# Kernel optimization log

Hardware: AMD Instinct MI355X
Metric: run time of the kernel (lower is better)

The kernel has to match this reference:

```python
import jax, jax.numpy as jnp
import numpy as np

B, F, V, E, D1, DD, L2 = 4096, 32, 50000, 64, 256, 16, 128


def setup_inputs() -> dict:
    key = jax.random.key(0)
    ks = jax.random.split(key, 16)
    s = 0.05  # small init scale to keep tanh unsaturated
    return {
        "sparse": jax.random.randint(ks[0], (B, F), 0, V, dtype=jnp.int32),
        "dense": jax.random.normal(ks[1], (B, DD), dtype=jnp.float32),
        "tables": jax.random.normal(ks[2], (F, V, E), dtype=jnp.float32) * s,
        "Wz": jax.random.normal(ks[3], (D1, F, E), dtype=jnp.float32) * s,
        "bz": jnp.zeros((D1,), jnp.float32),
        "Wpi": jax.random.normal(ks[4], (D1, F, F), dtype=jnp.float32) * s,
        "bpi": jnp.zeros((D1,), jnp.float32),
        "Wpo": jax.random.normal(ks[5], (D1, E, E), dtype=jnp.float32) * s,
        "bpo": jnp.zeros((D1,), jnp.float32),
        "B1": jax.random.normal(ks[6], (D1,), dtype=jnp.float32) * s,
        "W1": jax.random.normal(ks[7], (D1 + DD, D1), dtype=jnp.float32) * s,
        "b1": jnp.zeros((D1,), jnp.float32),
        "W2": jax.random.normal(ks[8], (D1, L2), dtype=jnp.float32) * s,
        "b2": jnp.zeros((L2,), jnp.float32),
        "W3": jax.random.normal(ks[9], (L2, 1), dtype=jnp.float32) * s,
        "b3": jnp.zeros((1,), jnp.float32),
    }


def reference(sparse, dense, tables, Wz, bz, Wpi, bpi, Wpo, bpo, B1,
              W1, b1, W2, b2, W3, b3):
    # Embedding lookup: per-field table gather -> [B, F, E]
    emb = tables[jnp.arange(F)[None, :], sparse]
    # Lz: Conv1d(in=F, kernel=E) over [B, F, E] == full contraction -> [B, D1]
    Lz = jnp.einsum('bfe,dfe->bd', emb, Wz) + bz
    # Inner product: [B, F, F], then Conv1d(in=F, kernel=F) full contraction
    inner = jnp.einsum('bie,bje->bij', emb, emb)
    Lp_inner = jnp.einsum('bij,dij->bd', inner, Wpi) + bpi
    # Outer product: sum_{i,j} x_i^T x_j == s^T s with s = sum_i x_i (exact rewrite)
    s = emb.sum(axis=1)                      # [B, E]
    outer = s[:, :, None] * s[:, None, :]    # [B, E, E]
    Lp_outer = jnp.einsum('bij,dij->bd', outer, Wpo) + bpo
    L1 = Lz + Lp_inner + Lp_outer + B1       # [B, D1]
    deep_x = jnp.concatenate([L1, dense], axis=1)  # [B, D1+DD]
    h = jnp.tanh(deep_x @ W1 + b1)
    h = jnp.tanh(h @ W2 + b2)
    out = (h @ W3 + b3)[:, 0]                # [B]
    return out
```

## Files before the change

### kernel.cpp

```cpp
#include <hip/hip_runtime.h>
#include <hip/hip_bf16.h>

#define B_    4096
#define F_    32
#define V_    50000
#define E_    64
#define D1_   256
#define DD_   16
#define L2N_  128
#define KX    3072
#define KTOT  7168
#define NKC   8

typedef __bf16 bf16x8 __attribute__((ext_vector_type(8)));
typedef float  f32x4  __attribute__((ext_vector_type(4)));

typedef __attribute__((address_space(1))) const void gvoid;
typedef __attribute__((address_space(3))) void svoid;

__device__ __forceinline__ ushort f2b(float f){
  __bf16 h = (__bf16)f; return __builtin_bit_cast(ushort, h);
}
__device__ __forceinline__ float b2f(ushort u){
  return __uint_as_float(((uint)u) << 16);
}
__device__ __forceinline__ float blo(uint u){ return __uint_as_float(u << 16); }
__device__ __forceinline__ float bhi(uint u){ return __uint_as_float(u & 0xffff0000u); }
__device__ __forceinline__ void gload16(const void* g, void* l){
  __builtin_amdgcn_global_load_lds((gvoid*)g, (svoid*)l, 16, 0, 0);
}

__global__ __launch_bounds__(256) void prep_gather(
    const float* __restrict__ Wz, const float* __restrict__ Wpi,
    const float* __restrict__ Wpo, const float* __restrict__ W1,
    const float* __restrict__ W2,
    const int* __restrict__ sparse, const float* __restrict__ tables,
    ushort* __restrict__ WBb, ushort* __restrict__ W1b, ushort* __restrict__ W2b,
    ushort* __restrict__ Xb, ushort* __restrict__ Sb) {
  __shared__ ushort gsh[4][32 * 72];
  int bid = blockIdx.x, t = threadIdx.x;
  if (bid < 640) {
    if (bid < 256) {
      int n = bid;
#pragma unroll
      for (int j = 0; j < 7; ++j) {
        int k4 = (j * 256 + t) * 4;
        float4 v;
        if (k4 < 2048)      v = *(const float4*)&Wz [(size_t)n * 2048 + k4];
        else if (k4 < 3072) v = *(const float4*)&Wpi[(size_t)n * 1024 + (k4 - 2048)];
        else                v = *(const float4*)&Wpo[(size_t)n * 4096 + (k4 - 3072)];
        ushort4 o = make_ushort4(f2b(v.x), f2b(v.y), f2b(v.z), f2b(v.w));
        *(ushort4*)&WBb[(size_t)n * KTOT + k4] = o;
      }
    } else if (bid < 512) {
      int n = bid - 256;
      float v0 = (t < 272) ? W1[(size_t)t * 256 + n] : 0.f;
      W1b[(size_t)n * 288 + t] = f2b(v0);
      if (t < 32) {
        int k2 = 256 + t;
        float v1 = (k2 < 272) ? W1[(size_t)k2 * 256 + n] : 0.f;
        W1b[(size_t)n * 288 + k2] = f2b(v1);
      }
    } else {
      int n = bid - 512;
      W2b[(size_t)n * 256 + t] = f2b(W2[(size_t)t * 128 + n]);
    }
    return;
  }

  int w = t >> 6, l = t & 63;
  int b = (bid - 640) * 4 + w;
  int fr = l & 15, q = l >> 4;

  int i0 = sparse[b * F_ + fr];
  int i1 = sparse[b * F_ + 16 + fr];
  const float* r0 = tables + ((size_t)fr * V_ + i0) * 64;
  const float* r1 = tables + ((size_t)(16 + fr) * V_ + i1) * 64;

  float4 v[2][2][2];
#pragma unroll
  for (int ks = 0; ks < 2; ++ks) {
    v[0][ks][0] = *(const float4*)(r0 + ks * 32 + q * 8);
    v[0][ks][1] = *(const float4*)(r0 + ks * 32 + q * 8 + 4);
    v[1][ks][0] = *(const float4*)(r1 + ks * 32 + q * 8);
    v[1][ks][1] = *(const float4*)(r1 + ks * 32 + q * 8 + 4);
  }

  bf16x8 fg[2][2];
#pragma unroll
  for (int rh = 0; rh < 2; ++rh)
#pragma unroll
    for (int ks = 0; ks < 2; ++ks) {
      bf16x8 a;
      a[0] = (__bf16)v[rh][ks][0].x; a[1] = (__bf16)v[rh][ks][0].y;
      a[2] = (__bf16)v[rh][ks][0].z; a[3] = (__bf16)v[rh][ks][0].w;
      a[4] = (__bf16)v[rh][ks][1].x; a[5] = (__bf16)v[rh][ks][1].y;
      a[6] = (__bf16)v[rh][ks][1].z; a[7] = (__bf16)v[rh][ks][1].w;
      fg[rh][ks] = a;
      *(bf16x8*)&Xb[(size_t)b * KX + (rh * 16 + fr) * 64 + ks * 32 + q * 8] = a;
    }

  float sv[2][8];
#pragma unroll
  for (int ks = 0; ks < 2; ++ks) {
    sv[ks][0] = v[0][ks][0].x + v[1][ks][0].x; sv[ks][1] = v[0][ks][0].y + v[1][ks][0].y;
    sv[ks][2] = v[0][ks][0].z + v[1][ks][0].z; sv[ks][3] = v[0][ks][0].w + v[1][ks][0].w;
    sv[ks][4] = v[0][ks][1].x + v[1][ks][1].x; sv[ks][5] = v[0][ks][1].y + v[1][ks][1].y;
    sv[ks][6] = v[0][ks][1].z + v[1][ks][1].z; sv[ks][7] = v[0][ks][1].w + v[1][ks][1].w;
  }
#pragma unroll
  for (int m = 1; m < 16; m <<= 1)
#pragma unroll
    for (int ks = 0; ks < 2; ++ks)
#pragma unroll
      for (int j = 0; j < 8; ++j)
        sv[ks][j] += __shfl_xor(sv[ks][j], m, 64);
  if (fr == 0) {
#pragma unroll
    for (int ks = 0; ks < 2; ++ks) {
      ushort4 o0 = make_ushort4(f2b(sv[ks][0]), f2b(sv[ks][1]), f2b(sv[ks][2]), f2b(sv[ks][3]));
      ushort4 o1 = make_ushort4(f2b(sv[ks][4]), f2b(sv[ks][5]), f2b(sv[ks][6]), f2b(sv[ks][7]));
      *(ushort4*)&Sb[(size_t)b * 64 + ks * 32 + q * 8]     = o0;
      *(ushort4*)&Sb[(size_t)b * 64 + ks * 32 + q * 8 + 4] = o1;
    }
  }

  f32x4 g[2][2] = {};
#pragma unroll
  for (int ks = 0; ks < 2; ++ks)
#pragma unroll
    for (int ri = 0; ri < 2; ++ri)
#pragma unroll
      for (int rj = 0; rj < 2; ++rj)
        g[ri][rj] = __builtin_amdgcn_mfma_f32_16x16x32_bf16(
            fg[ri][ks], fg[rj][ks], g[ri][rj], 0, 0, 0);

#pragma unroll
  for (int ri = 0; ri < 2; ++ri)
#pragma unroll
    for (int rj = 0; rj < 2; ++rj)
#pragma unroll
      for (int r = 0; r < 4; ++r)
        gsh[w][(ri * 16 + q * 4 + r) * 72 + rj * 16 + fr] = f2b(g[ri][rj][r]);
  {
    int rrow = l >> 1, rcol = (l & 1) * 16;
    uint4 ga = *(const uint4*)&gsh[w][rrow * 72 + rcol];
    uint4 gb = *(const uint4*)&gsh[w][rrow * 72 + rcol + 8];
    size_t dst = (size_t)b * KX + 2048 + rrow * 32 + rcol;
    *(uint4*)&Xb[dst]     = ga;
    *(uint4*)&Xb[dst + 8] = gb;
  }
}

__global__ __launch_bounds__(512, 1) void gemm_l1(
    const ushort* __restrict__ Xb, const ushort* __restrict__ WBb,
    const ushort* __restrict__ Sb, ushort* __restrict__ Lp) {
  __shared__ __align__(16) ushort As[2][128 * 64];
  __shared__ __align__(16) ushort Bs[2][256 * 64];
  __shared__ ushort Ssl[128 * 18];

  int bid = blockIdx.x;
  int kc  = bid & 7;
  int mT  = bid >> 3;
  int bRow = mT * 128;
  int kt0 = kc * 14;
  int i_start = min(max(0, kt0 - 48), 48);

  int tid = threadIdx.x, w = tid >> 6, l = tid & 63;
  int wm = (w >> 2) * 64, wn = (w & 3) * 64;
  int fr = l & 15, q = l >> 4;

#pragma unroll
  for (int r = 0; r < 2; ++r) {
    int p = r * 1024 + tid * 2;
    int row = p >> 4, col = p & 15;
    *(ushort2*)&Ssl[row * 18 + col] =
        *(const ushort2*)&Sb[(size_t)(bRow + row) * 64 + i_start + col];
  }

  uint4 sregu[4][2];
#pragma unroll
  for (int mi = 0; mi < 4; ++mi) {
    int grow = bRow + wm + mi * 16 + fr;
    sregu[mi][0] = *(const uint4*)&Sb[(size_t)grow * 64 + q * 8];
    sregu[mi][1] = *(const uint4*)&Sb[(size_t)grow * 64 + 32 + q * 8];
  }

  int r8 = l >> 3;
  int sg = ((l & 7) ^ r8) * 8;

  auto stageA = [&](int bI, int kt) {
    const ushort* src = Xb + (size_t)(bRow + w * 16 + r8) * KX + kt * 64 + sg;
#pragma unroll
    for (int c = 0; c < 2; ++c)
      gload16(src + (size_t)(c * 8) * KX, &As[bI][(w * 16 + c * 8) * 64]);
  };
  auto stageB = [&](int bI, int kt) {
    const ushort* src = WBb + (size_t)(w * 32 + r8) * KTOT + kt * 64 + sg;
#pragma unroll
    for (int c = 0; c < 4; ++c)
      gload16(src + (size_t)(c * 8) * KTOT, &Bs[bI][(w * 32 + c * 8) * 64]);
  };

  f32x4 acc[4][4] = {};
  bf16x8 af[4][2], bfr[4][2];
  int buf = 0;

  if (kt0 < 48) stageA(0, kt0);
  stageB(0, kt0);
  __syncthreads();

#pragma unroll
  for (int tl = 0; tl < 14; ++tl) {
    int kt = kt0 + tl;
    if (tl + 1 < 14) {
      if (kt + 1 < 48) stageA(buf ^ 1, kt + 1);
      stageB(buf ^ 1, kt + 1);
    }

#pragma unroll
    for (int ni = 0; ni < 4; ++ni) {
      int col = wn + ni * 16 + fr;
#pragma unroll
      for (int ks = 0; ks < 2; ++ks) {
        int slot = (ks * 4 + q) ^ (col & 7);
        bfr[ni][ks] = *(const bf16x8*)&Bs[buf][col * 64 + slot * 8];
      }
    }
    if (kt < 48) {
#pragma unroll
      for (int mi = 0; mi < 4; ++mi) {
        int row = wm + mi * 16 + fr;
#pragma unroll
        for (int ks = 0; ks < 2; ++ks) {
          int slot = (ks * 4 + q) ^ (row & 7);
          af[mi][ks] = *(const bf16x8*)&As[buf][row * 64 + slot * 8];
        }
      }
    } else {
      int iloc = kt - 48 - i_start;
#pragma unroll
      for (int mi = 0; mi < 4; ++mi) {
        float si = b2f(Ssl[(wm + mi * 16 + fr) * 18 + iloc]);
#pragma unroll
        for (int ks = 0; ks < 2; ++ks) {
          uint4 uv = sregu[mi][ks];
          bf16x8 a;
          a[0] = (__bf16)(si * blo(uv.x)); a[1] = (__bf16)(si * bhi(uv.x));
          a[2] = (__bf16)(si * blo(uv.y)); a[3] = (__bf16)(si * bhi(uv.y));
          a[4] = (__bf16)(si * blo(uv.z)); a[5] = (__bf16)(si * bhi(uv.z));
          a[6] = (__bf16)(si * blo(uv.w)); a[7] = (__bf16)(si * bhi(uv.w));
          af[mi][ks] = a;
        }
      }
    }
#pragma unroll
    for (int ks = 0; ks < 2; ++ks)
#pragma unroll
      for (int mi = 0; mi < 4; ++mi)
#pragma unroll
        for (int ni = 0; ni < 4; ++ni)
          acc[mi][ni] = __builtin_amdgcn_mfma_f32_16x16x32_bf16(
              af[mi][ks], bfr[ni][ks], acc[mi][ni], 0, 0, 0);
    __syncthreads();
    buf ^= 1;
  }

  ushort* Lpk = Lp + (size_t)kc * (B_ * D1_);
#pragma unroll
  for (int mi = 0; mi < 4; ++mi) {
    int row0 = bRow + wm + mi * 16 + q * 4;
#pragma unroll
    for (int ni = 0; ni < 4; ++ni) {
      int col = wn + ni * 16 + fr;
#pragma unroll
      for (int r = 0; r < 4; ++r)
        Lpk[(size_t)(row0 + r) * D1_ + col] = f2b(acc[mi][ni][r]);
    }
  }
}

__global__ __launch_bounds__(256) void mlp_fused(
    const ushort* __restrict__ Lp, const float* __restrict__ dense,
    const ushort* __restrict__ W1b, const ushort* __restrict__ W2b,
    const float* __restrict__ bz, const float* __restrict__ bpi,
    const float* __restrict__ bpo, const float* __restrict__ B1v,
    const float* __restrict__ b1, const float* __restrict__ b2,
    const float* __restrict__ W3, const float* __restrict__ b3,
    float* __restrict__ out) {
  __shared__ ushort hs[16 * 264];
  __shared__ ushort h2s[16 * 136];
  __shared__ float bvs[256];
  int b0 = blockIdx.x * 16;
  int tid = threadIdx.x, w = tid >> 6, l = tid & 63;
  int row = l & 15, q = l >> 4;
  int wn = w * 64;

  bvs[tid] = bz[tid] + bpi[tid] + bpo[tid] + B1v[tid];
  __syncthreads();

  f32x4 acc1[4] = {};
  for (int kt = 0; kt < 9; ++kt) {
    int k0 = kt * 32 + q * 8;
    bf16x8 afr;
    if (kt < 8) {
      size_t base = (size_t)(b0 + row) * D1_ + k0;
      float s[8] = {0.f, 0.f, 0.f, 0.f, 0.f, 0.f, 0.f, 0.f};
#pragma unroll
      for (int p = 0; p < NKC; ++p) {
        uint4 u = *(const uint4*)&Lp[(size_t)p * (B_ * D1_) + base];
        s[0] += blo(u.x); s[1] += bhi(u.x);
        s[2] += blo(u.y); s[3] += bhi(u.y);
        s[4] += blo(u.z); s[5] += bhi(u.z);
        s[6] += blo(u.w); s[7] += bhi(u.w);
      }
      float4 bv0 = *(const float4*)&bvs[k0];
      float4 bv1 = *(const float4*)&bvs[k0 + 4];
      afr[0] = (__bf16)(s[0] + bv0.x); afr[1] = (__bf16)(s[1] + bv0.y);
      afr[2] = (__bf16)(s[2] + bv0.z); afr[3] = (__bf16)(s[3] + bv0.w);
      afr[4] = (__bf16)(s[4] + bv1.x); afr[5] = (__bf16)(s[5] + bv1.y);
      afr[6] = (__bf16)(s[6] + bv1.z); afr[7] = (__bf16)(s[7] + bv1.w);
    } else if (q < 2) {
      float4 u0 = *(const float4*)&dense[(size_t)(b0 + row) * DD_ + q * 8];
      float4 u1 = *(const float4*)&dense[(size_t)(b0 + row) * DD_ + q * 8 + 4];
      afr[0] = (__bf16)u0.x; afr[1] = (__bf16)u0.y; afr[2] = (__bf16)u0.z; afr[3] = (__bf16)u0.w;
      afr[4] = (__bf16)u1.x; afr[5] = (__bf16)u1.y; afr[6] = (__bf16)u1.z; afr[7] = (__bf16)u1.w;
    } else {
      afr = (bf16x8)(__bf16)0.f;
    }
#pragma unroll
    for (int ni = 0; ni < 4; ++ni) {
      bf16x8 bfr = *(const bf16x8*)&W1b[(size_t)(wn + ni * 16 + row) * 288 + k0];
      acc1[ni] = __builtin_amdgcn_mfma_f32_16x16x32_bf16(afr, bfr, acc1[ni], 0, 0, 0);
    }
  }
#pragma unroll
  for (int ni = 0; ni < 4; ++ni) {
    int col = wn + ni * 16 + row;
    float bias = b1[col];
#pragma unroll
    for (int r = 0; r < 4; ++r)
      hs[(q * 4 + r) * 264 + col] = f2b(tanhf(acc1[ni][r] + bias));
  }
  __syncthreads();

  int wn2 = w * 32;
  f32x4 acc2[2] = {};
  for (int kt = 0; kt < 8; ++kt) {
    int k0 = kt * 32 + q * 8;
    bf16x8 afr = *(const bf16x8*)&hs[row * 264 + k0];
#pragma unroll
    for (int ni = 0; ni < 2; ++ni) {
      bf16x8 bfr = *(const bf16x8*)&W2b[(size_t)(wn2 + ni * 16 + row) * 256 + k0];
      acc2[ni] = __builtin_amdgcn_mfma_f32_16x16x32_bf16(afr, bfr, acc2[ni], 0, 0, 0);
    }
  }
#pragma unroll
  for (int ni = 0; ni < 2; ++ni) {
    int col = wn2 + ni * 16 + row;
    float bias = b2[col];
#pragma unroll
    for (int r = 0; r < 4; ++r)
      h2s[(q * 4 + r) * 136 + col] = f2b(tanhf(acc2[ni][r] + bias));
  }
  __syncthreads();

  if (w == 0) {
    int rr = l >> 2, g = l & 3;
    float sum = 0.f;
#pragma unroll
    for (int jj = 0; jj < 32; ++jj) {
      int j = g * 32 + jj;
      sum += b2f(h2s[rr * 136 + j]) * W3[j];
    }
    sum += __shfl_xor(sum, 1, 64);
    sum += __shfl_xor(sum, 2, 64);
    if (g == 0) out[b0 + rr] = sum + b3[0];
  }
}

extern "C" void kernel_launch(void* const* d_in, const int* in_sizes, int n_in,
                              void* d_out, int out_size, void* d_ws, size_t ws_size,
                              hipStream_t stream) {
  const int*   sparse = (const int*)  d_in[0];
  const float* dense  = (const float*)d_in[1];
  const float* tables = (const float*)d_in[2];
  const float* Wz     = (const float*)d_in[3];
  const float* bz     = (const float*)d_in[4];
  const float* Wpi    = (const float*)d_in[5];
  const float* bpi    = (const float*)d_in[6];
  const float* Wpo    = (const float*)d_in[7];
  const float* bpo    = (const float*)d_in[8];
  const float* B1v    = (const float*)d_in[9];
  const float* W1     = (const float*)d_in[10];
  const float* b1     = (const float*)d_in[11];
  const float* W2     = (const float*)d_in[12];
  const float* b2     = (const float*)d_in[13];
  const float* W3     = (const float*)d_in[14];
  const float* b3     = (const float*)d_in[15];
  float* out = (float*)d_out;

  char* ws = (char*)d_ws;
  ushort* Xb  = (ushort*)(ws);
  ushort* WBb = (ushort*)(ws + 25165824);
  ushort* W1b = (ushort*)(ws + 28835840);
  ushort* W2b = (ushort*)(ws + 28983296);
  ushort* Sb  = (ushort*)(ws + 29048832);
  ushort* Lp  = (ushort*)(ws + 29573120);

  prep_gather<<<dim3(1664), dim3(256), 0, stream>>>(
      Wz, Wpi, Wpo, W1, W2, sparse, tables, WBb, W1b, W2b, Xb, Sb);
  gemm_l1    <<<dim3(256),  dim3(512), 0, stream>>>(Xb, WBb, Sb, Lp);
  mlp_fused  <<<dim3(256),  dim3(256), 0, stream>>>(
      Lp, dense, W1b, W2b, bz, bpi, bpo, B1v, b1, b2, W3, b3, out);
}
```

Baseline: 59.77 us.

## Fuse MLP into split-K GEMM using per-tile atomic counter barrier

```diff
diff --git a/kernel.cpp b/kernel.cpp
--- a/kernel.cpp
+++ b/kernel.cpp
@@ -36,12 +36,14 @@
     const float* __restrict__ W2,
     const int* __restrict__ sparse, const float* __restrict__ tables,
     ushort* __restrict__ WBb, ushort* __restrict__ W1b, ushort* __restrict__ W2b,
-    ushort* __restrict__ Xb, ushort* __restrict__ Sb) {
+    ushort* __restrict__ Xb, ushort* __restrict__ Sb, int* __restrict__ cnt) {
   __shared__ ushort gsh[4][32 * 72];
   int bid = blockIdx.x, t = threadIdx.x;
-  if (bid < 640) {
-    if (bid < 256) {
-      int n = bid;
+  if (bid >= 1024) {
+    int bid2 = bid - 1024;
+    if (bid2 == 0 && t < 32) cnt[t] = 0;
+    if (bid2 < 256) {
+      int n = bid2;
 #pragma unroll
       for (int j = 0; j < 7; ++j) {
         int k4 = (j * 256 + t) * 4;
@@ -52,8 +54,8 @@
         ushort4 o = make_ushort4(f2b(v.x), f2b(v.y), f2b(v.z), f2b(v.w));
         *(ushort4*)&WBb[(size_t)n * KTOT + k4] = o;
       }
-    } else if (bid < 512) {
-      int n = bid - 256;
+    } else if (bid2 < 512) {
+      int n = bid2 - 256;
       float v0 = (t < 272) ? W1[(size_t)t * 256 + n] : 0.f;
       W1b[(size_t)n * 288 + t] = f2b(v0);
       if (t < 32) {
@@ -62,14 +64,14 @@
         W1b[(size_t)n * 288 + k2] = f2b(v1);
       }
     } else {
-      int n = bid - 512;
+      int n = bid2 - 512;
       W2b[(size_t)n * 256 + t] = f2b(W2[(size_t)t * 128 + n]);
     }
     return;
   }
 
   int w = t >> 6, l = t & 63;
-  int b = (bid - 640) * 4 + w;
+  int b = bid * 4 + w;
   int fr = l & 15, q = l >> 4;
 
   int i0 = sparse[b * F_ + fr];
@@ -152,9 +154,16 @@
   }
 }
 
-__global__ __launch_bounds__(512, 1) void gemm_l1(
+__global__ __launch_bounds__(512, 1) void gemm_mlp(
     const ushort* __restrict__ Xb, const ushort* __restrict__ WBb,
-    const ushort* __restrict__ Sb, ushort* __restrict__ Lp) {
+    const ushort* __restrict__ Sb, ushort* __restrict__ Lp,
+    const float* __restrict__ dense,
+    const ushort* __restrict__ W1b, const ushort* __restrict__ W2b,
+    const float* __restrict__ bz, const float* __restrict__ bpi,
+    const float* __restrict__ bpo, const float* __restrict__ B1v,
+    const float* __restrict__ b1, const float* __restrict__ b2,
+    const float* __restrict__ W3, const float* __restrict__ b3,
+    int* __restrict__ cnt, float* __restrict__ out) {
   __shared__ __align__(16) ushort As[2][128 * 64];
   __shared__ __align__(16) ushort Bs[2][256 * 64];
   __shared__ ushort Ssl[128 * 18];
@@ -278,104 +287,103 @@
         Lpk[(size_t)(row0 + r) * D1_ + col] = f2b(acc[mi][ni][r]);
     }
   }
-}
-
-__global__ __launch_bounds__(256) void mlp_fused(
-    const ushort* __restrict__ Lp, const float* __restrict__ dense,
-    const ushort* __restrict__ W1b, const ushort* __restrict__ W2b,
-    const float* __restrict__ bz, const float* __restrict__ bpi,
-    const float* __restrict__ bpo, const float* __restrict__ B1v,
-    const float* __restrict__ b1, const float* __restrict__ b2,
-    const float* __restrict__ W3, const float* __restrict__ b3,
-    float* __restrict__ out) {
-  __shared__ ushort hs[16 * 264];
-  __shared__ ushort h2s[16 * 136];
-  __shared__ float bvs[256];
-  int b0 = blockIdx.x * 16;
-  int tid = threadIdx.x, w = tid >> 6, l = tid & 63;
-  int row = l & 15, q = l >> 4;
-  int wn = w * 64;
-
-  bvs[tid] = bz[tid] + bpi[tid] + bpo[tid] + B1v[tid];
+
+  __threadfence();
+  if (tid == 0) {
+    atomicAdd(&cnt[mT], 1);
+    while (__hip_atomic_load(&cnt[mT], __ATOMIC_RELAXED,
+                             __HIP_MEMORY_SCOPE_AGENT) < NKC)
+      __builtin_amdgcn_s_sleep(8);
+  }
   __syncthreads();
-
-  f32x4 acc1[4] = {};
-  for (int kt = 0; kt < 9; ++kt) {
-    int k0 = kt * 32 + q * 8;
-    bf16x8 afr;
-    if (kt < 8) {
-      size_t base = (size_t)(b0 + row) * D1_ + k0;
-      float s[8] = {0.f, 0.f, 0.f, 0.f, 0.f, 0.f, 0.f, 0.f};
-#pragma unroll
-      for (int p = 0; p < NKC; ++p) {
-        uint4 u = *(const uint4*)&Lp[(size_t)p * (B_ * D1_) + base];
-        s[0] += blo(u.x); s[1] += bhi(u.x);
-        s[2] += blo(u.y); s[3] += bhi(u.y);
-        s[4] += blo(u.z); s[5] += bhi(u.z);
-        s[6] += blo(u.w); s[7] += bhi(u.w);
-      }
-      float4 bv0 = *(const float4*)&bvs[k0];
-      float4 bv1 = *(const float4*)&bvs[k0 + 4];
-      afr[0] = (__bf16)(s[0] + bv0.x); afr[1] = (__bf16)(s[1] + bv0.y);
-      afr[2] = (__bf16)(s[2] + bv0.z); afr[3] = (__bf16)(s[3] + bv0.w);
-      afr[4] = (__bf16)(s[4] + bv1.x); afr[5] = (__bf16)(s[5] + bv1.y);
-      afr[6] = (__bf16)(s[6] + bv1.z); afr[7] = (__bf16)(s[7] + bv1.w);
-    } else if (q < 2) {
-      float4 u0 = *(const float4*)&dense[(size_t)(b0 + row) * DD_ + q * 8];
-      float4 u1 = *(const float4*)&dense[(size_t)(b0 + row) * DD_ + q * 8 + 4];
-      afr[0] = (__bf16)u0.x; afr[1] = (__bf16)u0.y; afr[2] = (__bf16)u0.z; afr[3] = (__bf16)u0.w;
-      afr[4] = (__bf16)u1.x; afr[5] = (__bf16)u1.y; afr[6] = (__bf16)u1.z; afr[7] = (__bf16)u1.w;
-    } else {
-      afr = (bf16x8)(__bf16)0.f;
-    }
-#pragma unroll
-    for (int ni = 0; ni < 4; ++ni) {
-      bf16x8 bfr = *(const bf16x8*)&W1b[(size_t)(wn + ni * 16 + row) * 288 + k0];
-      acc1[ni] = __builtin_amdgcn_mfma_f32_16x16x32_bf16(afr, bfr, acc1[ni], 0, 0, 0);
-    }
-  }
-#pragma unroll
-  for (int ni = 0; ni < 4; ++ni) {
-    int col = wn + ni * 16 + row;
-    float bias = b1[col];
-#pragma unroll
-    for (int r = 0; r < 4; ++r)
-      hs[(q * 4 + r) * 264 + col] = f2b(tanhf(acc1[ni][r] + bias));
-  }
-  __syncthreads();
-
-  int wn2 = w * 32;
-  f32x4 acc2[2] = {};
-  for (int kt = 0; kt < 8; ++kt) {
-    int k0 = kt * 32 + q * 8;
-    bf16x8 afr = *(const bf16x8*)&hs[row * 264 + k0];
+  __threadfence();
+
+  {
+    ushort* hs  = &As[0][0];
+    ushort* h2s = &As[0][0] + 16 * 264;
+    float*  bvs = (float*)(&As[0][0] + 16 * 264 + 16 * 136);
+
+    int b0 = bRow + kc * 16;
+    int row = fr;
+
+    if (tid < 256) bvs[tid] = bz[tid] + bpi[tid] + bpo[tid] + B1v[tid];
+    __syncthreads();
+
+    int wn1 = w * 32;
+    f32x4 acc1[2] = {};
+    for (int kt = 0; kt < 9; ++kt) {
+      int k0 = kt * 32 + q * 8;
+      bf16x8 afr;
+      if (kt < 8) {
+        size_t base = (size_t)(b0 + row) * D1_ + k0;
+        float s[8] = {0.f, 0.f, 0.f, 0.f, 0.f, 0.f, 0.f, 0.f};
+#pragma unroll
+        for (int p = 0; p < NKC; ++p) {
+          uint4 u = *(const uint4*)&Lp[(size_t)p * (B_ * D1_) + base];
+          s[0] += blo(u.x); s[1] += bhi(u.x);
+          s[2] += blo(u.y); s[3] += bhi(u.y);
+          s[4] += blo(u.z); s[5] += bhi(u.z);
+          s[6] += blo(u.w); s[7] += bhi(u.w);
+        }
+        float4 bv0 = *(const float4*)&bvs[k0];
+        float4 bv1 = *(const float4*)&bvs[k0 + 4];
+        afr[0] = (__bf16)(s[0] + bv0.x); afr[1] = (__bf16)(s[1] + bv0.y);
+        afr[2] = (__bf16)(s[2] + bv0.z); afr[3] = (__bf16)(s[3] + bv0.w);
+        afr[4] = (__bf16)(s[4] + bv1.x); afr[5] = (__bf16)(s[5] + bv1.y);
+        afr[6] = (__bf16)(s[6] + bv1.z); afr[7] = (__bf16)(s[7] + bv1.w);
+      } else if (q < 2) {
+        float4 u0 = *(const float4*)&dense[(size_t)(b0 + row) * DD_ + q * 8];
+        float4 u1 = *(const float4*)&dense[(size_t)(b0 + row) * DD_ + q * 8 + 4];
+        afr[0] = (__bf16)u0.x; afr[1] = (__bf16)u0.y; afr[2] = (__bf16)u0.z; afr[3] = (__bf16)u0.w;
+        afr[4] = (__bf16)u1.x; afr[5] = (__bf16)u1.y; afr[6] = (__bf16)u1.z; afr[7] = (__bf16)u1.w;
+      } else {
+        afr = (bf16x8)(__bf16)0.f;
+      }
+#pragma unroll
+      for (int ni = 0; ni < 2; ++ni) {
+        bf16x8 bfr2 = *(const bf16x8*)&W1b[(size_t)(wn1 + ni * 16 + row) * 288 + k0];
+        acc1[ni] = __builtin_amdgcn_mfma_f32_16x16x32_bf16(afr, bfr2, acc1[ni], 0, 0, 0);
+      }
+    }
 #pragma unroll
     for (int ni = 0; ni < 2; ++ni) {
-      bf16x8 bfr = *(const bf16x8*)&W2b[(size_t)(wn2 + ni * 16 + row) * 256 + k0];
-      acc2[ni] = __builtin_amdgcn_mfma_f32_16x16x32_bf16(afr, bfr, acc2[ni], 0, 0, 0);
-    }
-  }
-#pragma unroll
-  for (int ni = 0; ni < 2; ++ni) {
-    int col = wn2 + ni * 16 + row;
-    float bias = b2[col];
-#pragma unroll
-    for (int r = 0; r < 4; ++r)
-      h2s[(q * 4 + r) * 136 + col] = f2b(tanhf(acc2[ni][r] + bias));
-  }
-  __syncthreads();
-
-  if (w == 0) {
-    int rr = l >> 2, g = l & 3;
-    float sum = 0.f;
-#pragma unroll
-    for (int jj = 0; jj < 32; ++jj) {
-      int j = g * 32 + jj;
-      sum += b2f(h2s[rr * 136 + j]) * W3[j];
-    }
-    sum += __shfl_xor(sum, 1, 64);
-    sum += __shfl_xor(sum, 2, 64);
-    if (g == 0) out[b0 + rr] = sum + b3[0];
+      int col = wn1 + ni * 16 + row;
+      float bias = b1[col];
+#pragma unroll
+      for (int r = 0; r < 4; ++r)
+        hs[(q * 4 + r) * 264 + col] = f2b(tanhf(acc1[ni][r] + bias));
+    }
+    __syncthreads();
+
+    int wn2 = w * 16;
+    f32x4 acc2 = {};
+    for (int kt = 0; kt < 8; ++kt) {
+      int k0 = kt * 32 + q * 8;
+      bf16x8 afr = *(const bf16x8*)&hs[row * 264 + k0];
+      bf16x8 bfr2 = *(const bf16x8*)&W2b[(size_t)(wn2 + row) * 256 + k0];
+      acc2 = __builtin_amdgcn_mfma_f32_16x16x32_bf16(afr, bfr2, acc2, 0, 0, 0);
+    }
+    {
+      int col = wn2 + row;
+      float bias = b2[col];
+#pragma unroll
+      for (int r = 0; r < 4; ++r)
+        h2s[(q * 4 + r) * 136 + col] = f2b(tanhf(acc2[r] + bias));
+    }
+    __syncthreads();
+
+    if (w == 0) {
+      int rr = l >> 2, g = l & 3;
+      float sum = 0.f;
+#pragma unroll
+      for (int jj = 0; jj < 32; ++jj) {
+        int j = g * 32 + jj;
+        sum += b2f(h2s[rr * 136 + j]) * W3[j];
+      }
+      sum += __shfl_xor(sum, 1, 64);
+      sum += __shfl_xor(sum, 2, 64);
+      if (g == 0) out[b0 + rr] = sum + b3[0];
+    }
   }
 }
 
@@ -407,10 +415,11 @@
   ushort* W2b = (ushort*)(ws + 28983296);
   ushort* Sb  = (ushort*)(ws + 29048832);
   ushort* Lp  = (ushort*)(ws + 29573120);
+  int*    cnt = (int*)   (ws + 46350336);
 
   prep_gather<<<dim3(1664), dim3(256), 0, stream>>>(
-      Wz, Wpi, Wpo, W1, W2, sparse, tables, WBb, W1b, W2b, Xb, Sb);
-  gemm_l1    <<<dim3(256),  dim3(512), 0, stream>>>(Xb, WBb, Sb, Lp);
-  mlp_fused  <<<dim3(256),  dim3(256), 0, stream>>>(
-      Lp, dense, W1b, W2b, bz, bpi, bpo, B1v, b1, b2, W3, b3, out);
-}
+      Wz, Wpi, Wpo, W1, W2, sparse, tables, WBb, W1b, W2b, Xb, Sb, cnt);
+  gemm_mlp   <<<dim3(256),  dim3(512), 0, stream>>>(
+      Xb, WBb, Sb, Lp, dense, W1b, W2b, bz, bpi, bpo, B1v,
+      b1, b2, W3, b3, cnt, out);
+}
```

New measurement: 169.7 us. 184% more time.

## Halve GEMM M-tile, cut K-split to four, map split-K chunks to XCDs

Applied to the files above, without the earlier changes.

```diff
diff --git a/kernel.cpp b/kernel.cpp
--- a/kernel.cpp
+++ b/kernel.cpp
@@ -10,7 +10,7 @@
 #define L2N_  128
 #define KX    3072
 #define KTOT  7168
-#define NKC   8
+#define NKC   4
 
 typedef __bf16 bf16x8 __attribute__((ext_vector_type(8)));
 typedef float  f32x4  __attribute__((ext_vector_type(4)));
@@ -39,9 +39,10 @@
     ushort* __restrict__ Xb, ushort* __restrict__ Sb) {
   __shared__ ushort gsh[4][32 * 72];
   int bid = blockIdx.x, t = threadIdx.x;
-  if (bid < 640) {
-    if (bid < 256) {
-      int n = bid;
+  if (bid >= 1024) {
+    int bid2 = bid - 1024;
+    if (bid2 < 256) {
+      int n = bid2;
 #pragma unroll
       for (int j = 0; j < 7; ++j) {
         int k4 = (j * 256 + t) * 4;
@@ -52,8 +53,8 @@
         ushort4 o = make_ushort4(f2b(v.x), f2b(v.y), f2b(v.z), f2b(v.w));
         *(ushort4*)&WBb[(size_t)n * KTOT + k4] = o;
       }
-    } else if (bid < 512) {
-      int n = bid - 256;
+    } else if (bid2 < 512) {
+      int n = bid2 - 256;
       float v0 = (t < 272) ? W1[(size_t)t * 256 + n] : 0.f;
       W1b[(size_t)n * 288 + t] = f2b(v0);
       if (t < 32) {
@@ -62,14 +63,14 @@
         W1b[(size_t)n * 288 + k2] = f2b(v1);
       }
     } else {
-      int n = bid - 512;
+      int n = bid2 - 512;
       W2b[(size_t)n * 256 + t] = f2b(W2[(size_t)t * 128 + n]);
     }
     return;
   }
 
   int w = t >> 6, l = t & 63;
-  int b = (bid - 640) * 4 + w;
+  int b = bid * 4 + w;
   int fr = l & 15, q = l >> 4;
 
   int i0 = sparse[b * F_ + fr];
@@ -155,32 +156,30 @@
 __global__ __launch_bounds__(512, 1) void gemm_l1(
     const ushort* __restrict__ Xb, const ushort* __restrict__ WBb,
     const ushort* __restrict__ Sb, ushort* __restrict__ Lp) {
-  __shared__ __align__(16) ushort As[2][128 * 64];
+  __shared__ __align__(16) ushort As[2][64 * 64];
   __shared__ __align__(16) ushort Bs[2][256 * 64];
-  __shared__ ushort Ssl[128 * 18];
+  __shared__ ushort Ssl[64 * 72];
 
   int bid = blockIdx.x;
-  int kc  = bid & 7;
-  int mT  = bid >> 3;
-  int bRow = mT * 128;
-  int kt0 = kc * 14;
-  int i_start = min(max(0, kt0 - 48), 48);
+  int xcd = bid & 7;
+  int kc  = xcd >> 1;
+  int mT  = (bid >> 3) * 2 + (xcd & 1);
+  int bRow = mT * 64;
+  int kt0 = kc * 28;
 
   int tid = threadIdx.x, w = tid >> 6, l = tid & 63;
-  int wm = (w >> 2) * 64, wn = (w & 3) * 64;
+  int wm = (w >> 2) * 32, wn = (w & 3) * 64;
   int fr = l & 15, q = l >> 4;
 
-#pragma unroll
-  for (int r = 0; r < 2; ++r) {
-    int p = r * 1024 + tid * 2;
-    int row = p >> 4, col = p & 15;
-    *(ushort2*)&Ssl[row * 18 + col] =
-        *(const ushort2*)&Sb[(size_t)(bRow + row) * 64 + i_start + col];
-  }
-
-  uint4 sregu[4][2];
-#pragma unroll
-  for (int mi = 0; mi < 4; ++mi) {
+  {
+    int p = tid * 8;
+    int row = p >> 6, col = p & 63;
+    *(uint4*)&Ssl[row * 72 + col] = *(const uint4*)&Sb[(size_t)(bRow + row) * 64 + col];
+  }
+
+  uint4 sregu[2][2];
+#pragma unroll
+  for (int mi = 0; mi < 2; ++mi) {
     int grow = bRow + wm + mi * 16 + fr;
     sregu[mi][0] = *(const uint4*)&Sb[(size_t)grow * 64 + q * 8];
     sregu[mi][1] = *(const uint4*)&Sb[(size_t)grow * 64 + 32 + q * 8];
@@ -190,10 +189,8 @@
   int sg = ((l & 7) ^ r8) * 8;
 
   auto stageA = [&](int bI, int kt) {
-    const ushort* src = Xb + (size_t)(bRow + w * 16 + r8) * KX + kt * 64 + sg;
-#pragma unroll
-    for (int c = 0; c < 2; ++c)
-      gload16(src + (size_t)(c * 8) * KX, &As[bI][(w * 16 + c * 8) * 64]);
+    const ushort* src = Xb + (size_t)(bRow + w * 8 + r8) * KX + kt * 64 + sg;
+    gload16(src, &As[bI][(w * 8) * 64]);
   };
   auto stageB = [&](int bI, int kt) {
     const ushort* src = WBb + (size_t)(w * 32 + r8) * KTOT + kt * 64 + sg;
@@ -202,8 +199,8 @@
       gload16(src + (size_t)(c * 8) * KTOT, &Bs[bI][(w * 32 + c * 8) * 64]);
   };
 
-  f32x4 acc[4][4] = {};
-  bf16x8 af[4][2], bfr[4][2];
+  f32x4 acc[2][4] = {};
+  bf16x8 af[2][2], bfr[4][2];
   int buf = 0;
 
   if (kt0 < 48) stageA(0, kt0);
@@ -211,9 +208,9 @@
   __syncthreads();
 
 #pragma unroll
-  for (int tl = 0; tl < 14; ++tl) {
+  for (int tl = 0; tl < 28; ++tl) {
     int kt = kt0 + tl;
-    if (tl + 1 < 14) {
+    if (tl + 1 < 28) {
       if (kt + 1 < 48) stageA(buf ^ 1, kt + 1);
       stageB(buf ^ 1, kt + 1);
     }
@@ -229,7 +226,7 @@
     }
     if (kt < 48) {
 #pragma unroll
-      for (int mi = 0; mi < 4; ++mi) {
+      for (int mi = 0; mi < 2; ++mi) {
         int row = wm + mi * 16 + fr;
 #pragma unroll
         for (int ks = 0; ks < 2; ++ks) {
@@ -238,10 +235,10 @@
         }
       }
     } else {
-      int iloc = kt - 48 - i_start;
-#pragma unroll
-      for (int mi = 0; mi < 4; ++mi) {
-        float si = b2f(Ssl[(wm + mi * 16 + fr) * 18 + iloc]);
+      int i = kt - 48;
+#pragma unroll
+      for (int mi = 0; mi < 2; ++mi) {
+        float si = b2f(Ssl[(wm + mi * 16 + fr) * 72 + i]);
 #pragma unroll
         for (int ks = 0; ks < 2; ++ks) {
           uint4 uv = sregu[mi][ks];
@@ -257,7 +254,7 @@
 #pragma unroll
     for (int ks = 0; ks < 2; ++ks)
 #pragma unroll
-      for (int mi = 0; mi < 4; ++mi)
+      for (int mi = 0; mi < 2; ++mi)
 #pragma unroll
         for (int ni = 0; ni < 4; ++ni)
           acc[mi][ni] = __builtin_amdgcn_mfma_f32_16x16x32_bf16(
@@ -268,7 +265,7 @@
 
   ushort* Lpk = Lp + (size_t)kc * (B_ * D1_);
 #pragma unroll
-  for (int mi = 0; mi < 4; ++mi) {
+  for (int mi = 0; mi < 2; ++mi) {
     int row0 = bRow + wm + mi * 16 + q * 4;
 #pragma unroll
     for (int ni = 0; ni < 4; ++ni) {
```

Result: slower. 61.95 us (+3.6%).

## Fuse embedding gather into GEMM A-staging instead of materializing bf16 embeddings

Applied to the files above, without the earlier changes.

```diff
diff --git a/kernel.cpp b/kernel.cpp
--- a/kernel.cpp
+++ b/kernel.cpp
@@ -8,7 +8,6 @@
 #define D1_   256
 #define DD_   16
 #define L2N_  128
-#define KX    3072
 #define KTOT  7168
 #define NKC   8
 
@@ -36,12 +35,13 @@
     const float* __restrict__ W2,
     const int* __restrict__ sparse, const float* __restrict__ tables,
     ushort* __restrict__ WBb, ushort* __restrict__ W1b, ushort* __restrict__ W2b,
-    ushort* __restrict__ Xb, ushort* __restrict__ Sb) {
+    ushort* __restrict__ Xg, ushort* __restrict__ Sb) {
   __shared__ ushort gsh[4][32 * 72];
   int bid = blockIdx.x, t = threadIdx.x;
-  if (bid < 640) {
-    if (bid < 256) {
-      int n = bid;
+  if (bid >= 1024) {
+    int bid2 = bid - 1024;
+    if (bid2 < 256) {
+      int n = bid2;
 #pragma unroll
       for (int j = 0; j < 7; ++j) {
         int k4 = (j * 256 + t) * 4;
@@ -52,8 +52,8 @@
         ushort4 o = make_ushort4(f2b(v.x), f2b(v.y), f2b(v.z), f2b(v.w));
         *(ushort4*)&WBb[(size_t)n * KTOT + k4] = o;
       }
-    } else if (bid < 512) {
-      int n = bid - 256;
+    } else if (bid2 < 512) {
+      int n = bid2 - 256;
       float v0 = (t < 272) ? W1[(size_t)t * 256 + n] : 0.f;
       W1b[(size_t)n * 288 + t] = f2b(v0);
       if (t < 32) {
@@ -62,14 +62,14 @@
         W1b[(size_t)n * 288 + k2] = f2b(v1);
       }
     } else {
-      int n = bid - 512;
+      int n = bid2 - 512;
       W2b[(size_t)n * 256 + t] = f2b(W2[(size_t)t * 128 + n]);
     }
     return;
   }
 
   int w = t >> 6, l = t & 63;
-  int b = (bid - 640) * 4 + w;
+  int b = bid * 4 + w;
   int fr = l & 15, q = l >> 4;
 
   int i0 = sparse[b * F_ + fr];
@@ -97,7 +97,6 @@
       a[4] = (__bf16)v[rh][ks][1].x; a[5] = (__bf16)v[rh][ks][1].y;
       a[6] = (__bf16)v[rh][ks][1].z; a[7] = (__bf16)v[rh][ks][1].w;
       fg[rh][ks] = a;
-      *(bf16x8*)&Xb[(size_t)b * KX + (rh * 16 + fr) * 64 + ks * 32 + q * 8] = a;
     }
 
   float sv[2][8];
@@ -146,18 +145,21 @@
     int rrow = l >> 1, rcol = (l & 1) * 16;
     uint4 ga = *(const uint4*)&gsh[w][rrow * 72 + rcol];
     uint4 gb = *(const uint4*)&gsh[w][rrow * 72 + rcol + 8];
-    size_t dst = (size_t)b * KX + 2048 + rrow * 32 + rcol;
-    *(uint4*)&Xb[dst]     = ga;
-    *(uint4*)&Xb[dst + 8] = gb;
+    size_t dst = (size_t)b * 1024 + rrow * 32 + rcol;
+    *(uint4*)&Xg[dst]     = ga;
+    *(uint4*)&Xg[dst + 8] = gb;
   }
 }
 
 __global__ __launch_bounds__(512, 1) void gemm_l1(
-    const ushort* __restrict__ Xb, const ushort* __restrict__ WBb,
-    const ushort* __restrict__ Sb, ushort* __restrict__ Lp) {
+    const ushort* __restrict__ Xg, const ushort* __restrict__ WBb,
+    const ushort* __restrict__ Sb,
+    const int* __restrict__ sparse, const float* __restrict__ tables,
+    ushort* __restrict__ Lp) {
   __shared__ __align__(16) ushort As[2][128 * 64];
   __shared__ __align__(16) ushort Bs[2][256 * 64];
   __shared__ ushort Ssl[128 * 18];
+  __shared__ int sidx[128 * 33];
 
   int bid = blockIdx.x;
   int kc  = bid & 7;
@@ -178,6 +180,15 @@
         *(const ushort2*)&Sb[(size_t)(bRow + row) * 64 + i_start + col];
   }
 
+  if (kt0 < 32) {
+    int row = tid >> 2, c = (tid & 3) * 8;
+    int4 a = *(const int4*)&sparse[(bRow + row) * F_ + c];
+    int4 b = *(const int4*)&sparse[(bRow + row) * F_ + c + 4];
+    int* d = &sidx[row * 33 + c];
+    d[0] = a.x; d[1] = a.y; d[2] = a.z; d[3] = a.w;
+    d[4] = b.x; d[5] = b.y; d[6] = b.z; d[7] = b.w;
+  }
+
   uint4 sregu[4][2];
 #pragma unroll
   for (int mi = 0; mi < 4; ++mi) {
@@ -185,15 +196,32 @@
     sregu[mi][0] = *(const uint4*)&Sb[(size_t)grow * 64 + q * 8];
     sregu[mi][1] = *(const uint4*)&Sb[(size_t)grow * 64 + 32 + q * 8];
   }
+  __syncthreads();
 
   int r8 = l >> 3;
   int sg = ((l & 7) ^ r8) * 8;
 
   auto stageA = [&](int bI, int kt) {
-    const ushort* src = Xb + (size_t)(bRow + w * 16 + r8) * KX + kt * 64 + sg;
-#pragma unroll
-    for (int c = 0; c < 2; ++c)
-      gload16(src + (size_t)(c * 8) * KX, &As[bI][(w * 16 + c * 8) * 64]);
+    if (kt < 32) {
+#pragma unroll
+      for (int h = 0; h < 2; ++h) {
+        int unit = tid + h * 512;
+        int row = unit >> 3, g = unit & 7;
+        const float* src =
+            tables + ((size_t)kt * V_ + sidx[row * 33 + kt]) * 64 + g * 8;
+        float4 u0 = *(const float4*)src;
+        float4 u1 = *(const float4*)(src + 4);
+        int slot = g ^ (row & 7);
+        ushort* d = &As[bI][row * 64 + slot * 8];
+        *(ushort4*)d       = make_ushort4(f2b(u0.x), f2b(u0.y), f2b(u0.z), f2b(u0.w));
+        *(ushort4*)(d + 4) = make_ushort4(f2b(u1.x), f2b(u1.y), f2b(u1.z), f2b(u1.w));
+      }
+    } else {
+      const ushort* src = Xg + (size_t)(bRow + w * 16 + r8) * 1024 + (kt - 32) * 64 + sg;
+#pragma unroll
+      for (int c = 0; c < 2; ++c)
+        gload16(src + (size_t)(c * 8) * 1024, &As[bI][(w * 16 + c * 8) * 64]);
+    }
   };
   auto stageB = [&](int bI, int kt) {
     const ushort* src = WBb + (size_t)(w * 32 + r8) * KTOT + kt * 64 + sg;
@@ -401,16 +429,16 @@
   float* out = (float*)d_out;
 
   char* ws = (char*)d_ws;
-  ushort* Xb  = (ushort*)(ws);
-  ushort* WBb = (ushort*)(ws + 25165824);
-  ushort* W1b = (ushort*)(ws + 28835840);
-  ushort* W2b = (ushort*)(ws + 28983296);
-  ushort* Sb  = (ushort*)(ws + 29048832);
-  ushort* Lp  = (ushort*)(ws + 29573120);
+  ushort* Xg  = (ushort*)(ws);
+  ushort* WBb = (ushort*)(ws + 8388608);
+  ushort* W1b = (ushort*)(ws + 12058624);
+  ushort* W2b = (ushort*)(ws + 12206080);
+  ushort* Sb  = (ushort*)(ws + 12271616);
+  ushort* Lp  = (ushort*)(ws + 12795904);
 
   prep_gather<<<dim3(1664), dim3(256), 0, stream>>>(
-      Wz, Wpi, Wpo, W1, W2, sparse, tables, WBb, W1b, W2b, Xb, Sb);
-  gemm_l1    <<<dim3(256),  dim3(512), 0, stream>>>(Xb, WBb, Sb, Lp);
+      Wz, Wpi, Wpo, W1, W2, sparse, tables, WBb, W1b, W2b, Xg, Sb);
+  gemm_l1    <<<dim3(256),  dim3(512), 0, stream>>>(Xg, WBb, Sb, sparse, tables, Lp);
   mlp_fused  <<<dim3(256),  dim3(256), 0, stream>>>(
       Lp, dense, W1b, W2b, bz, bpi, bpo, B1v, b1, b2, W3, b3, out);
 }
```

After: 63.02 us. +5.4%, slower.
